# Performance work log

Measured on AMD Instinct MI355X. Metric: run time of the kernel, lower is better.

## Reference

```python
import jax, jax.numpy as jnp
import numpy as np

GAMMA = 0.5
EPS = 1e-06
REL_THRESH = 1e-09


def setup_inputs() -> dict:
    key = jax.random.key(0)
    k1, k2 = jax.random.split(key)
    B, T, D = 4, 4096, 256
    A_rel = jax.random.uniform(k1, (B, T, T), dtype=jnp.float32)
    # symmetrize as the docstring states A_rel is symmetric
    A_rel = 0.5 * (A_rel + jnp.swapaxes(A_rel, -1, -2))
    k_seq = jax.random.normal(k2, (B, T, D), dtype=jnp.float32)
    return {"A_rel": A_rel, "k_seq": k_seq}


def reference(A_rel, k_seq):
    # init_sequence: symmetric normalization W = D^{-1/2} A D^{-1/2}
    D = jnp.sum(A_rel, axis=-1) + EPS                  # (B, T)
    d_inv_sqrt = 1.0 / jnp.sqrt(D)                     # (B, T)
    W = A_rel * d_inv_sqrt[:, :, None] * d_inv_sqrt[:, None, :]  # (B, T, T)

    T = A_rel.shape[1]
    # step t uses W[:, t, :t+1] -> lower-triangular (incl. diagonal) causal mask
    tril = jnp.tril(jnp.ones((T, T), dtype=W.dtype))   # (T, T)
    W_causal = W * tril                                # (B, T, T)

    # a_t = sum_{s<=t} W[b,t,s] * k_s  for every t at once
    a = jnp.einsum('bts,bsd->btd', W_causal, k_seq)    # (B, T, D)

    # has_relation[b,t] = max_{s<=t} |W[b,t,s]| > 1e-9
    has_relation = jnp.max(jnp.abs(W) * tril, axis=-1) > REL_THRESH  # (B, T)

    a_scaled = a * jnp.sqrt(jnp.asarray(GAMMA, dtype=a.dtype))
    out = a_scaled * has_relation[:, :, None].astype(a_scaled.dtype)
    return out
```

## Files before the change

### kernel.cpp

```cpp
#include <hip/hip_runtime.h>
#include <hip/hip_bf16.h>

constexpr int Bn = 4;
constexpr int Tn = 4096;
constexpr int Dn = 256;
constexpr int NT = Tn / 64;
constexpr int NTRI = NT * (NT + 1) / 2;

using ushort = unsigned short;
typedef short short8 __attribute__((ext_vector_type(8)));
typedef float f32x4 __attribute__((ext_vector_type(4)));

__device__ __forceinline__ ushort f2bu(float f) {
    __hip_bfloat16 h = __float2bfloat16(f);
    return __builtin_bit_cast(unsigned short, h);
}
__device__ __forceinline__ void gld_lds16(const ushort* g, ushort* l) {
    __builtin_amdgcn_global_load_lds((const __attribute__((address_space(1))) void*)g,
                                     (__attribute__((address_space(3))) void*)l,
                                     16, 0, 0);
}

__global__ __launch_bounds__(256) void rowsum_convert_kernel(
    const float* __restrict__ A, float* __restrict__ dis, ushort* __restrict__ Apk) {
    int r = blockIdx.x;
    int b = r >> 12;
    int t = r & (Tn - 1);
    int it = t >> 6, m = t & 63;
    const float* row = A + (size_t)r * Tn;
    ushort* tb = Apk + (size_t)b * NTRI * 4096 + (size_t)(it * (it + 1) / 2) * 4096 + m * 64;
    int tid = threadIdx.x;
    float s = 0.f;
#pragma unroll
    for (int q = 0; q < 2; ++q) {
        int g = q * 256 + tid;
        int c0 = g * 8;
        float4 v0 = *(const float4*)(row + c0);
        float4 v1 = *(const float4*)(row + c0 + 4);
        s += v0.x + v0.y + v0.z + v0.w + v1.x + v1.y + v1.z + v1.w;
        int kt = g >> 3;
        if (kt <= it) {
            float f[8] = {v0.x, v0.y, v0.z, v0.w, v1.x, v1.y, v1.z, v1.w};
            int c = c0 & 63;
            if (kt == it) {
#pragma unroll
                for (int j = 0; j < 8; ++j)
                    if (c + j > m) f[j] = 0.f;
            }
            unsigned w[4];
#pragma unroll
            for (int e = 0; e < 4; ++e)
                w[e] = (unsigned)f2bu(f[2 * e]) | ((unsigned)f2bu(f[2 * e + 1]) << 16);
            *(uint4*)(tb + (size_t)kt * 4096 + c) = make_uint4(w[0], w[1], w[2], w[3]);
        }
    }
#pragma unroll
    for (int k = 1; k < 64; k <<= 1) s += __shfl_xor(s, k, 64);
    __shared__ float ws[4];
    if ((tid & 63) == 0) ws[tid >> 6] = s;
    __syncthreads();
    if (tid == 0) {
        float tot = ws[0] + ws[1] + ws[2] + ws[3];
        dis[r] = rsqrtf(tot + 1e-6f);
    }
}

__global__ __launch_bounds__(256) void scale_transpose_kernel(
    const float* __restrict__ K, const float* __restrict__ dis, ushort* __restrict__ kT) {
    int bid = blockIdx.x;
    int b = bid >> 8;
    int rr = bid & 255;
    int st = rr >> 2, dt = rr & 3;
    int s0 = st * 64, d0 = dt * 64;
    __shared__ ushort tile[64][72];
    int tid = threadIdx.x;
#pragma unroll
    for (int q = 0; q < 2; ++q) {
        int idx = q * 256 + tid;
        int sl = idx >> 3, dl0 = (idx & 7) * 8;
        const float* g = K + ((size_t)(b * Tn + s0 + sl) * Dn + d0 + dl0);
        float sc = dis[b * Tn + s0 + sl];
        float4 v0 = *(const float4*)g;
        float4 v1 = *(const float4*)(g + 4);
        tile[sl][dl0 + 0] = f2bu(v0.x * sc);
        tile[sl][dl0 + 1] = f2bu(v0.y * sc);
        tile[sl][dl0 + 2] = f2bu(v0.z * sc);
        tile[sl][dl0 + 3] = f2bu(v0.w * sc);
        tile[sl][dl0 + 4] = f2bu(v1.x * sc);
        tile[sl][dl0 + 5] = f2bu(v1.y * sc);
        tile[sl][dl0 + 6] = f2bu(v1.z * sc);
        tile[sl][dl0 + 7] = f2bu(v1.w * sc);
    }
    __syncthreads();
#pragma unroll
    for (int q = 0; q < 2; ++q) {
        int idx = q * 256 + tid;
        int dl = idx >> 3, sl0 = (idx & 7) * 8;
        unsigned w[4];
#pragma unroll
        for (int e = 0; e < 4; ++e) {
            unsigned lo = tile[sl0 + 2 * e][dl];
            unsigned hi = tile[sl0 + 2 * e + 1][dl];
            w[e] = lo | (hi << 16);
        }
        *(uint4*)(kT + ((size_t)(b * Dn + d0 + dl) * Tn + s0 + sl0)) =
            make_uint4(w[0], w[1], w[2], w[3]);
    }
}

constexpr int BM = 64, BN = 128, BK = 64;

__global__ __launch_bounds__(256) void gemm_causal_kernel(
    const ushort* __restrict__ Apk, const ushort* __restrict__ kT,
    const float* __restrict__ dis, float* __restrict__ out) {
    __shared__ __attribute__((aligned(16))) ushort As[BM * BK];
    __shared__ __attribute__((aligned(16))) ushort Bs[BN * BK];
    __shared__ float rs[BM];

    int bid = blockIdx.x;
    int it = 63 - (bid >> 3);
    int sub = bid & 7;
    int b = sub >> 1;
    int d0 = (sub & 1) * BN;
    int t0 = it * BM;

    int tid = threadIdx.x;
    int lane = tid & 63;
    int w = tid >> 6;
    int l15 = lane & 15;
    int kq = (lane >> 4) * 8;

    const ushort* Atri = Apk + (size_t)b * NTRI * 4096 + (size_t)(it * (it + 1) / 2) * 4096;
    const size_t kTbase = (size_t)(b * Dn + d0) * Tn;

    if (tid < BM) rs[tid] = 0.70710678118654752f * dis[b * Tn + t0 + tid];

    f32x4 acc[2][4];
#pragma unroll
    for (int mi = 0; mi < 2; ++mi)
#pragma unroll
        for (int ni = 0; ni < 4; ++ni) acc[mi][ni] = (f32x4){0.f, 0.f, 0.f, 0.f};

    int mrow = (w >> 1) * 32;
    int ncol = (w & 1) * 64;

    int nkt = it + 1;
    for (int kt = 0; kt < nkt; ++kt) {
#pragma unroll
        for (int q = 0; q < 2; ++q) {
            int idx = q * 256 + tid;
            gld_lds16(Atri + (size_t)kt * 4096 + idx * 8, As + idx * 8);
        }
        int s0 = kt * BK;
#pragma unroll
        for (int q = 0; q < 4; ++q) {
            int idx = q * 256 + tid;
            int n = idx >> 3, sc = (idx & 7) * 8;
            gld_lds16(kT + kTbase + (size_t)n * Tn + s0 + sc, Bs + idx * 8);
        }
        __syncthreads();

#pragma unroll
        for (int ki = 0; ki < 2; ++ki) {
            int kc = ki * 32 + kq;
            short8 af[2];
#pragma unroll
            for (int mi = 0; mi < 2; ++mi)
                af[mi] = *(const short8*)&As[(mrow + 16 * mi + l15) * BK + kc];
            short8 bfr[4];
#pragma unroll
            for (int ni = 0; ni < 4; ++ni)
                bfr[ni] = *(const short8*)&Bs[(ncol + 16 * ni + l15) * BK + kc];
#pragma unroll
            for (int mi = 0; mi < 2; ++mi)
#pragma unroll
                for (int ni = 0; ni < 4; ++ni)
                    acc[mi][ni] = __builtin_amdgcn_mfma_f32_16x16x32_bf16(
                        af[mi], bfr[ni], acc[mi][ni], 0, 0, 0);
        }
        __syncthreads();
    }

#pragma unroll
    for (int mi = 0; mi < 2; ++mi) {
#pragma unroll
        for (int ni = 0; ni < 4; ++ni) {
            int tl = mrow + 16 * mi + (lane >> 4) * 4;
            int d = d0 + ncol + 16 * ni + l15;
#pragma unroll
            for (int r = 0; r < 4; ++r) {
                int t = t0 + tl + r;
                out[(size_t)(b * Tn + t) * Dn + d] = acc[mi][ni][r] * rs[tl + r];
            }
        }
    }
}

extern "C" void kernel_launch(void* const* d_in, const int* in_sizes, int n_in,
                              void* d_out, int out_size, void* d_ws, size_t ws_size,
                              hipStream_t stream) {
    const float* A = (const float*)d_in[0];
    const float* K = (const float*)d_in[1];
    float* out = (float*)d_out;

    float* dis = (float*)d_ws;
    ushort* kT = (ushort*)(dis + Bn * Tn);
    ushort* Apk = kT + (size_t)Bn * Dn * Tn;

    rowsum_convert_kernel<<<dim3(Bn * Tn), dim3(256), 0, stream>>>(A, dis, Apk);
    scale_transpose_kernel<<<dim3(Bn * (Tn / 64) * (Dn / 64)), dim3(256), 0, stream>>>(K, dis, kT);
    gemm_causal_kernel<<<dim3(NT * 2 * Bn), dim3(256), 0, stream>>>(Apk, kT, dis, out);
}
```

Measured before the change: 455.6 us.

## Double-buffer GEMM LDS tiles and halve N tile for more blocks

The causal GEMM now stages the next K tile into a second LDS buffer while computing on the current one, overlapping global-to-LDS loads with MFMA work. The N tile shrinks from 128 to 64 columns, doubling the grid so the triangular workload spreads over more CUs. In exchange, A tiles are loaded twice as often and each block does less MFMA work per load.

Measured after the change: 448.8 us. About the same (-1.5%).

```diff
diff --git a/kernel.cpp b/kernel.cpp
--- a/kernel.cpp
+++ b/kernel.cpp
@@ -108,21 +108,21 @@
     }
 }
 
-constexpr int BM = 64, BN = 128, BK = 64;
+constexpr int BK = 64;
 
 __global__ __launch_bounds__(256) void gemm_causal_kernel(
     const ushort* __restrict__ Apk, const ushort* __restrict__ kT,
     const float* __restrict__ dis, float* __restrict__ out) {
-    __shared__ __attribute__((aligned(16))) ushort As[BM * BK];
-    __shared__ __attribute__((aligned(16))) ushort Bs[BN * BK];
-    __shared__ float rs[BM];
+    __shared__ __attribute__((aligned(16))) ushort As[2][64 * BK];
+    __shared__ __attribute__((aligned(16))) ushort Bs[2][64 * BK];
+    __shared__ float rs[64];
 
     int bid = blockIdx.x;
-    int it = 63 - (bid >> 3);
-    int sub = bid & 7;
-    int b = sub >> 1;
-    int d0 = (sub & 1) * BN;
-    int t0 = it * BM;
+    int it = 63 - (bid >> 4);
+    int sub = bid & 15;
+    int b = sub >> 2;
+    int d0 = (sub & 3) * 64;
+    int t0 = it * 64;
 
     int tid = threadIdx.x;
     int lane = tid & 63;
@@ -133,48 +133,53 @@
     const ushort* Atri = Apk + (size_t)b * NTRI * 4096 + (size_t)(it * (it + 1) / 2) * 4096;
     const size_t kTbase = (size_t)(b * Dn + d0) * Tn;
 
-    if (tid < BM) rs[tid] = 0.70710678118654752f * dis[b * Tn + t0 + tid];
-
-    f32x4 acc[2][4];
+    if (tid < 64) rs[tid] = 0.70710678118654752f * dis[b * Tn + t0 + tid];
+
+    f32x4 acc[2][2];
 #pragma unroll
     for (int mi = 0; mi < 2; ++mi)
 #pragma unroll
-        for (int ni = 0; ni < 4; ++ni) acc[mi][ni] = (f32x4){0.f, 0.f, 0.f, 0.f};
+        for (int ni = 0; ni < 2; ++ni) acc[mi][ni] = (f32x4){0.f, 0.f, 0.f, 0.f};
 
     int mrow = (w >> 1) * 32;
-    int ncol = (w & 1) * 64;
-
+    int ncol = (w & 1) * 32;
     int nkt = it + 1;
-    for (int kt = 0; kt < nkt; ++kt) {
+
+    auto stage = [&](int buf, int kt) {
 #pragma unroll
         for (int q = 0; q < 2; ++q) {
             int idx = q * 256 + tid;
-            gld_lds16(Atri + (size_t)kt * 4096 + idx * 8, As + idx * 8);
-        }
-        int s0 = kt * BK;
-#pragma unroll
-        for (int q = 0; q < 4; ++q) {
+            gld_lds16(Atri + (size_t)kt * 4096 + idx * 8, &As[buf][idx * 8]);
+        }
+#pragma unroll
+        for (int q = 0; q < 2; ++q) {
             int idx = q * 256 + tid;
             int n = idx >> 3, sc = (idx & 7) * 8;
-            gld_lds16(kT + kTbase + (size_t)n * Tn + s0 + sc, Bs + idx * 8);
-        }
-        __syncthreads();
-
+            gld_lds16(kT + kTbase + (size_t)n * Tn + kt * BK + sc, &Bs[buf][idx * 8]);
+        }
+    };
+
+    stage(0, 0);
+    __syncthreads();
+
+    for (int kt = 0; kt < nkt; ++kt) {
+        int cur = kt & 1;
+        if (kt + 1 < nkt) stage(cur ^ 1, kt + 1);
 #pragma unroll
         for (int ki = 0; ki < 2; ++ki) {
             int kc = ki * 32 + kq;
             short8 af[2];
 #pragma unroll
             for (int mi = 0; mi < 2; ++mi)
-                af[mi] = *(const short8*)&As[(mrow + 16 * mi + l15) * BK + kc];
-            short8 bfr[4];
-#pragma unroll
-            for (int ni = 0; ni < 4; ++ni)
-                bfr[ni] = *(const short8*)&Bs[(ncol + 16 * ni + l15) * BK + kc];
+                af[mi] = *(const short8*)&As[cur][(mrow + 16 * mi + l15) * BK + kc];
+            short8 bfr[2];
+#pragma unroll
+            for (int ni = 0; ni < 2; ++ni)
+                bfr[ni] = *(const short8*)&Bs[cur][(ncol + 16 * ni + l15) * BK + kc];
 #pragma unroll
             for (int mi = 0; mi < 2; ++mi)
 #pragma unroll
-                for (int ni = 0; ni < 4; ++ni)
+                for (int ni = 0; ni < 2; ++ni)
                     acc[mi][ni] = __builtin_amdgcn_mfma_f32_16x16x32_bf16(
                         af[mi], bfr[ni], acc[mi][ni], 0, 0, 0);
         }
@@ -184,7 +189,7 @@
 #pragma unroll
     for (int mi = 0; mi < 2; ++mi) {
 #pragma unroll
-        for (int ni = 0; ni < 4; ++ni) {
+        for (int ni = 0; ni < 2; ++ni) {
             int tl = mrow + 16 * mi + (lane >> 4) * 4;
             int d = d0 + ncol + 16 * ni + l15;
 #pragma unroll
@@ -209,5 +214,5 @@
 
     rowsum_convert_kernel<<<dim3(Bn * Tn), dim3(256), 0, stream>>>(A, dis, Apk);
     scale_transpose_kernel<<<dim3(Bn * (Tn / 64) * (Dn / 64)), dim3(256), 0, stream>>>(K, dis, kT);
-    gemm_causal_kernel<<<dim3(NT * 2 * Bn), dim3(256), 0, stream>>>(Apk, kT, dis, out);
-}
+    gemm_causal_kernel<<<dim3(NT * 16), dim3(256), 0, stream>>>(Apk, kT, dis, out);
+}
```
